# Kernel tuning notes

Measured on AMD Instinct MI355X. Metric: run time of the kernel, lower is better.

The kernel has to match this reference:

```python
import jax, jax.numpy as jnp
import numpy as np

B = 256
NUM_PRIMARY = 32      # cfg.num_primary_caps
PRIM_ATOMS = 8
NUM_CLASSES = 10
DIGIT_ATOMS = 16
NUM_ROUTING = 3       # cfg.num_routing (DigitCap)
IN_DIM = 6 * 6 * NUM_PRIMARY  # 1152
NUM_PIXELS = 28 * 28 * 1


def squash(s, axis):
    # v = ||s||^2/(1+||s||^2) * s/||s||
    n2 = jnp.sum(jnp.square(s), axis=axis, keepdims=True)
    return s * (n2 / (1.0 + n2)) / jnp.sqrt(n2 + 1e-9)


def conv2d(x, w, stride):
    return jax.lax.conv_general_dilated(
        x, w, (stride, stride), 'VALID',
        dimension_numbers=('NCHW', 'OIHW', 'NCHW'))


def setup_inputs() -> dict:
    key = jax.random.key(0)
    ks = jax.random.split(key, 10)
    x = jax.random.uniform(ks[0], (B, 1, 28, 28), jnp.float32)
    labels = jax.random.randint(ks[1], (B,), 0, NUM_CLASSES)
    y = jax.nn.one_hot(labels, NUM_CLASSES, dtype=jnp.float32)
    conv1_w = 0.05 * jax.random.normal(ks[2], (256, 1, 9, 9), jnp.float32)
    conv1_b = jnp.full((256,), 0.1, jnp.float32)
    # primary capsule conv: 256 -> 32 caps * 8 atoms, k=9, s=2 (bias applied after routing)
    prim_w = 0.05 * jax.random.normal(ks[3], (NUM_PRIMARY * PRIM_ATOMS, 256, 9, 9), jnp.float32)
    prim_b = jnp.full((NUM_PRIMARY, PRIM_ATOMS), 0.1, jnp.float32)
    # digit capsule transform: [in_dim, in_atoms, out_dim, out_atoms]
    digit_w = 0.05 * jax.random.normal(ks[4], (IN_DIM, PRIM_ATOMS, NUM_CLASSES, DIGIT_ATOMS), jnp.float32)
    digit_b = jnp.full((NUM_CLASSES, DIGIT_ATOMS), 0.1, jnp.float32)
    w1 = 0.05 * jax.random.normal(ks[5], (NUM_CLASSES * DIGIT_ATOMS, 512), jnp.float32)
    b1 = jnp.zeros((512,), jnp.float32)
    w2 = 0.05 * jax.random.normal(ks[6], (512, 1024), jnp.float32)
    b2 = jnp.zeros((1024,), jnp.float32)
    w3 = 0.05 * jax.random.normal(ks[7], (1024, NUM_PIXELS), jnp.float32)
    b3 = jnp.zeros((NUM_PIXELS,), jnp.float32)
    return dict(x=x, y=y, conv1_w=conv1_w, conv1_b=conv1_b, prim_w=prim_w,
                prim_b=prim_b, digit_w=digit_w, digit_b=digit_b,
                w1=w1, b1=b1, w2=w2, b2=b2, w3=w3, b3=b3)


def reference(x, y, conv1_w, conv1_b, prim_w, prim_b, digit_w, digit_b,
              w1, b1, w2, b2, w3, b3):
    # conv stem
    h = jax.nn.relu(conv2d(x, conv1_w, 1) + conv1_b[None, :, None, None])  # [B,256,20,20]

    # PrimaryCap: conv votes [B, in_dim=1, out=32, atoms=8, 6, 6]; num_routing=1
    votes_p = conv2d(h, prim_w, 2).reshape(B, NUM_PRIMARY, PRIM_ATOMS, 6, 6)
    # one routing iter, input_dim=1: softmax(zeros) over output_dim -> uniform 1/32
    preact_p = votes_p / NUM_PRIMARY + prim_b[None, :, :, None, None]
    caps1 = squash(preact_p, axis=2)  # [B,32,8,6,6]

    # permute(0,1,3,4,2) then flatten -> [B, 1152, 8]
    x3 = jnp.transpose(caps1, (0, 1, 3, 4, 2)).reshape(B, IN_DIM, PRIM_ATOMS)

    # DigitCap votes: [B, in_dim, out_dim, out_atoms]
    votes = jnp.einsum('bia,iaot->biot', x3, digit_w)
    logits = jnp.zeros((B, IN_DIM, NUM_CLASSES), votes.dtype)
    act = None
    for _ in range(NUM_ROUTING):
        route = jax.nn.softmax(logits, axis=2)  # over output capsules
        preact = jnp.einsum('bio,biot->bot', route, votes) + digit_b
        act = squash(preact, axis=-1)  # [B,10,16]
        logits = logits + jnp.einsum('biot,bot->bio', votes, act)
    digit = act

    # Reconstruction: mask by label, 160 -> 512 -> 1024 -> 784
    masked = (digit * y[:, :, None]).reshape(B, NUM_CLASSES * DIGIT_ATOMS)
    r = jax.nn.relu(masked @ w1 + b1)
    r = jax.nn.relu(r @ w2 + b2)
    recon = jax.nn.sigmoid(r @ w3 + b3)
    return digit, recon
```

## Files before the change

kernel.cpp:

```cpp
#include <hip/hip_runtime.h>
#include <hip/hip_bf16.h>

typedef unsigned short u16;
typedef unsigned int u32;

static __device__ __forceinline__ float us2f(u16 u) {
    return __uint_as_float(((u32)u) << 16);
}
static __device__ __forceinline__ u16 f2bu(float f) {
    u32 u = __float_as_uint(f);
    return (u16)((u + 0x7fffu + ((u >> 16) & 1u)) >> 16);
}

typedef __attribute__((ext_vector_type(8))) __bf16 bf16x8;
typedef __attribute__((ext_vector_type(4))) float f32x4;

static __device__ __forceinline__ void async16(const u16* g, u16* l) {
    __builtin_amdgcn_global_load_lds(
        (const __attribute__((address_space(1))) unsigned int*)g,
        (__attribute__((address_space(3))) unsigned int*)l, 16, 0, 0);
}

__global__ void fill_sentinel(float* out, int n, float val) {
    int g = blockIdx.x * 256 + threadIdx.x;
    if (g < n) out[g] = val;
}

__global__ __launch_bounds__(256) void conv_c1wb(const float* __restrict__ w,
                                                 u16* __restrict__ wb)
{
    const int j = blockIdx.x, c = threadIdx.x;
    wb[j * 256 + c] = f2bu(w[c * 81 + j]);
}

__global__ __launch_bounds__(256) void conv1_kernel(const float* __restrict__ x,
    const u16* __restrict__ wb, const float* __restrict__ bias, u16* __restrict__ h)
{
    __shared__ float xs[784];
    __shared__ u16 wl[81 * 256];
    const int b = blockIdx.x >> 2, g = blockIdx.x & 3;
    const int c = threadIdx.x;
    for (int idx = c; idx < 784; idx += 256) xs[idx] = x[b * 784 + idx];
    for (int idx = c; idx < 20736; idx += 256) wl[idx] = wb[idx];
    __syncthreads();
    const float bv = bias[c];
    #pragma unroll 1
    for (int iy = g * 5; iy < g * 5 + 5; ++iy) {
        float acc[20];
        #pragma unroll
        for (int i = 0; i < 20; ++i) acc[i] = bv;
        #pragma unroll 1
        for (int dy = 0; dy < 9; ++dy) {
            float xr[28];
            const float4* xrow = reinterpret_cast<const float4*>(&xs[(iy + dy) * 28]);
            #pragma unroll
            for (int i = 0; i < 7; ++i) {
                float4 v = xrow[i];
                xr[4*i] = v.x; xr[4*i+1] = v.y; xr[4*i+2] = v.z; xr[4*i+3] = v.w;
            }
            #pragma unroll
            for (int dx = 0; dx < 9; ++dx) {
                const float wv = us2f(wl[(dy * 9 + dx) * 256 + c]);
                #pragma unroll
                for (int ix = 0; ix < 20; ++ix) acc[ix] += xr[ix + dx] * wv;
            }
        }
        u16* hp = h + ((b * 20 + iy) * 20) * 256 + c;
        #pragma unroll
        for (int ix = 0; ix < 20; ++ix) hp[ix * 256] = f2bu(fmaxf(acc[ix], 0.f));
    }
}

__global__ __launch_bounds__(256) void transpose_primw(const float* __restrict__ w,
                                                       u16* __restrict__ wt)
{
    __shared__ u16 wl[81 * 258];
    const int n = blockIdx.x, tid = threadIdx.x;
    const float* ws = w + (size_t)n * 20736;
    for (int idx = tid; idx < 20736; idx += 256) {
        const int cc = idx / 81, kk = idx - cc * 81;
        wl[kk * 258 + cc] = f2bu(ws[idx]);
    }
    __syncthreads();
    u16* wo = wt + (size_t)n * 20736;
    for (int q = tid; q < 20736; q += 256)
        wo[q] = wl[(q >> 8) * 258 + (q & 255)];
}

__global__ __launch_bounds__(256) void conv_dwb(const float* __restrict__ dw,
                                                u16* __restrict__ dwb_t)
{
    const int g = blockIdx.x * 256 + threadIdx.x;
    dwb_t[g] = f2bu(dw[g]);
}

__global__ __launch_bounds__(256) void prim_gemm_split(const u16* __restrict__ h,
    const u16* __restrict__ wT, float* __restrict__ pm)
{
    __shared__ u16 As[128 * 32];
    __shared__ u16 Bs[128 * 32];
    const int tid = threadIdx.x;
    const int split = blockIdx.y;
    const int mt = blockIdx.x % 72, nt = blockIdx.x / 72;
    const int mBase = mt * 128, nBase = nt * 128;
    const int tq = tid & 3, tr = tid >> 2;
    const int swzq = tq ^ ((tr >> 1) & 3);
    int m0 = mBase + tr;
    int b0 = m0 / 36, r0 = m0 % 36;
    int aBase0 = ((b0 * 20 + 2 * (r0 / 6)) * 20 + 2 * (r0 % 6)) * 256 + swzq * 8;
    int m1 = m0 + 64;
    int b1 = m1 / 36, r1 = m1 % 36;
    int aBase1 = ((b1 * 20 + 2 * (r1 / 6)) * 20 + 2 * (r1 % 6)) * 256 + swzq * 8;
    const int bBase0 = (nBase + tr) * 20736 + swzq * 8;
    const int bBase1 = (nBase + tr + 64) * 20736 + swzq * 8;
    int kglob = split * 1728;
    int ky = kglob / 2304; int krem = kglob - ky * 2304;
    int kx = krem >> 8; int c0 = krem & 255;

    f32x4 acc[4][4];
    #pragma unroll
    for (int i = 0; i < 4; ++i)
        #pragma unroll
        for (int j = 0; j < 4; ++j) acc[i][j] = (f32x4){0.f, 0.f, 0.f, 0.f};

    const int lane = tid & 63;
    const int wvi = tid >> 6; const int wm = wvi >> 1, wn = wvi & 1;
    const int lcol = lane & 15, lquad = lane >> 4;
    u16* asDst0 = As + wvi * 512;
    u16* asDst1 = As + 2048 + wvi * 512;
    u16* bsDst0 = Bs + wvi * 512;
    u16* bsDst1 = Bs + 2048 + wvi * 512;
    const int rswz = (lquad ^ ((lcol >> 1) & 3)) * 8;
    const u16* Arow = As + (wm * 64 + lcol) * 32 + rswz;
    const u16* Brow = Bs + (wn * 64 + lcol) * 32 + rswz;

    #pragma unroll 1
    for (int kt = 0; kt < 54; ++kt) {
        const int koffA = (ky * 20 + kx) * 256 + c0;
        async16(h + aBase0 + koffA, asDst0);
        async16(h + aBase1 + koffA, asDst1);
        async16(wT + bBase0 + kglob, bsDst0);
        async16(wT + bBase1 + kglob, bsDst1);
        __syncthreads();
        bf16x8 af[4], bfr[4];
        #pragma unroll
        for (int i = 0; i < 4; ++i)
            af[i] = *reinterpret_cast<const bf16x8*>(Arow + i * 512);
        #pragma unroll
        for (int j = 0; j < 4; ++j)
            bfr[j] = *reinterpret_cast<const bf16x8*>(Brow + j * 512);
        #pragma unroll
        for (int i = 0; i < 4; ++i)
            #pragma unroll
            for (int j = 0; j < 4; ++j)
                acc[i][j] = __builtin_amdgcn_mfma_f32_16x16x32_bf16(af[i], bfr[j], acc[i][j], 0, 0, 0);
        kglob += 32; c0 += 32;
        if (c0 == 256) { c0 = 0; if (++kx == 9) { kx = 0; ++ky; } }
        __syncthreads();
    }
    #pragma unroll
    for (int i = 0; i < 4; ++i) {
        const int mrow = mBase + wm * 64 + i * 16 + (lane >> 4) * 4;
        #pragma unroll
        for (int j = 0; j < 4; ++j) {
            const int ncol = nBase + wn * 64 + j * 16 + lcol;
            #pragma unroll
            for (int r = 0; r < 4; ++r)
                unsafeAtomicAdd(&pm[(size_t)(mrow + r) * 256 + ncol], acc[i][j][r]);
        }
    }
}

__global__ __launch_bounds__(256) void squash_kernel(float* __restrict__ pm,
    const float* __restrict__ pb)
{
    const int m = blockIdx.x, t = threadIdx.x;
    float pre = pm[(size_t)m * 256 + t] * (1.f / 32.f) + pb[t];
    float sq = pre * pre;
    sq += __shfl_xor(sq, 1); sq += __shfl_xor(sq, 2); sq += __shfl_xor(sq, 4);
    float scale = (sq / (1.f + sq)) * rsqrtf(sq + 1e-9f);
    pm[(size_t)m * 256 + t] = pre * scale;
}

__global__ __launch_bounds__(192) void votes_gemm(const float* __restrict__ x3m,
    const u16* __restrict__ dwb_t, u16* __restrict__ votes, int hb)
{
    __shared__ float dws[8 * 1280];
    __shared__ float x3s[64 * 64];
    const int ic = blockIdx.x * 8, bc = blockIdx.y * 64;
    const int tid = threadIdx.x;
    for (int q = tid; q < 10240; q += 192)
        dws[q] = us2f(dwb_t[(size_t)ic * 1280 + q]);
    for (int q = tid; q < 4096; q += 192) {
        const int b_l = q >> 6, r = q & 63, i_l = r >> 3, a = r & 7;
        const int i = ic + i_l, cap = i / 36, p = i - cap * 36;
        x3s[q] = x3m[((size_t)(hb + bc + b_l) * 36 + p) * 256 + cap * 8 + a];
    }
    __syncthreads();
    if (tid < 160) {
        const int ot = tid;
        float dwr[8][8];
        #pragma unroll
        for (int i_l = 0; i_l < 8; ++i_l)
            #pragma unroll
            for (int a = 0; a < 8; ++a)
                dwr[i_l][a] = dws[i_l * 1280 + a * 160 + ot];
        #pragma unroll 1
        for (int b_l = 0; b_l < 64; ++b_l) {
            u16 ob[8];
            #pragma unroll
            for (int i_l = 0; i_l < 8; ++i_l) {
                const float* xp = &x3s[b_l * 64 + i_l * 8];
                float v = 0.f;
                #pragma unroll
                for (int a = 0; a < 8; ++a) v += xp[a] * dwr[i_l][a];
                ob[i_l] = f2bu(v);
            }
            uint4 o4;
            o4.x = (u32)ob[0] | ((u32)ob[1] << 16);
            o4.y = (u32)ob[2] | ((u32)ob[3] << 16);
            o4.z = (u32)ob[4] | ((u32)ob[5] << 16);
            o4.w = (u32)ob[6] | ((u32)ob[7] << 16);
            *reinterpret_cast<uint4*>(&votes[((size_t)(bc + b_l) * 160 + ot) * 1152 + ic]) = o4;
        }
    }
}

__global__ __launch_bounds__(256) void routing_act3(const u16* __restrict__ votes,
    const float* __restrict__ logits, float* __restrict__ preactD, int hb, int uniform)
{
    __shared__ float route_s[384 * 10];
    __shared__ float vs[160 * 65];
    const int ic = blockIdx.x * 384, b_l = blockIdx.y;
    const int gb = hb + b_l;
    const int tid = threadIdx.x;
    if (!uniform) {
        for (int q = tid; q < 384; q += 256) {
            const float* lg = &logits[((size_t)gb * 1152 + ic + q) * 10];
            float l[10]; float mx = -1e30f;
            #pragma unroll
            for (int k = 0; k < 10; ++k) { l[k] = lg[k]; mx = fmaxf(mx, l[k]); }
            float s = 0.f;
            #pragma unroll
            for (int k = 0; k < 10; ++k) { l[k] = __expf(l[k] - mx); s += l[k]; }
            const float inv = 1.f / s;
            #pragma unroll
            for (int k = 0; k < 10; ++k) route_s[q * 10 + k] = l[k] * inv;
        }
    }
    float acc = 0.f;
    const int o = (tid & 255) >> 4;
    #pragma unroll 1
    for (int sc = 0; sc < 6; ++sc) {
        __syncthreads();
        for (int q = tid; q < 1280; q += 256) {
            const int ot = q >> 3, i8 = q & 7;
            const uint4 d = *reinterpret_cast<const uint4*>(
                &votes[((size_t)b_l * 160 + ot) * 1152 + ic + sc * 64 + i8 * 8]);
            const u32 du[4] = {d.x, d.y, d.z, d.w};
            float* vp = &vs[ot * 65 + i8 * 8];
            #pragma unroll
            for (int k = 0; k < 4; ++k) {
                vp[2 * k]     = __uint_as_float(du[k] << 16);
                vp[2 * k + 1] = __uint_as_float(du[k] & 0xffff0000u);
            }
        }
        __syncthreads();
        if (tid < 160) {
            const float* vrow = &vs[tid * 65];
            if (uniform) {
                float s = 0.f;
                #pragma unroll
                for (int il = 0; il < 64; ++il) s += vrow[il];
                acc += 0.1f * s;
            } else {
                const float* rp = &route_s[sc * 640 + o];
                #pragma unroll
                for (int il = 0; il < 64; ++il)
                    acc += rp[il * 10] * vrow[il];
            }
        }
    }
    if (tid < 160)
        unsafeAtomicAdd(&preactD[(size_t)gb * 160 + tid], acc);
}

__global__ __launch_bounds__(192) void routing_squash(const float* __restrict__ preactD,
    const float* __restrict__ db, float* __restrict__ act, float* __restrict__ dout, int hb)
{
    const int b = hb + blockIdx.x, tid = threadIdx.x;
    if (tid < 160) {
        float pre = preactD[(size_t)b * 160 + tid] + db[tid];
        float sq = pre * pre;
        sq += __shfl_xor(sq, 1); sq += __shfl_xor(sq, 2);
        sq += __shfl_xor(sq, 4); sq += __shfl_xor(sq, 8);
        float scale = (sq / (1.f + sq)) * rsqrtf(sq + 1e-9f);
        float a = pre * scale;
        act[(size_t)b * 160 + tid] = a;
        if (dout) dout[(size_t)b * 160 + tid] = a;
    }
}

__global__ __launch_bounds__(128) void routing_upd3(const u16* __restrict__ votes,
    const float* __restrict__ act, float* __restrict__ logits, int hb, int first)
{
    __shared__ float act_s[160];
    const int b_l = blockIdx.y, gb = hb + b_l;
    const int i = blockIdx.x * 128 + threadIdx.x;
    for (int q = threadIdx.x; q < 160; q += 128)
        act_s[q] = act[(size_t)gb * 160 + q];
    __syncthreads();
    float acc[10];
    #pragma unroll
    for (int k = 0; k < 10; ++k) acc[k] = 0.f;
    const u16* vb = &votes[(size_t)b_l * 160 * 1152 + i];
    #pragma unroll
    for (int ot = 0; ot < 160; ++ot)
        acc[ot >> 4] += us2f(vb[(size_t)ot * 1152]) * act_s[ot];
    float* lp = &logits[((size_t)gb * 1152 + i) * 10];
    if (first) {
        #pragma unroll
        for (int k = 0; k < 10; ++k) lp[k] = acc[k];
    } else {
        #pragma unroll
        for (int k = 0; k < 10; ++k) lp[k] += acc[k];
    }
}

__global__ __launch_bounds__(256) void mlp_layer(const float* __restrict__ in,
    const float* __restrict__ maskY, const float* __restrict__ w,
    const float* __restrict__ bias, float* __restrict__ outp, int K, int N, int mode)
{
    __shared__ float ins[4 * 1024];
    const int b0 = blockIdx.x * 4;
    const int n = blockIdx.y * 256 + threadIdx.x;
    for (int idx = threadIdx.x; idx < 4 * K; idx += 256) {
        float v = in[(size_t)b0 * K + idx];
        if (maskY) {
            const int b_l = idx / K, j = idx % K;
            v *= maskY[(b0 + b_l) * 10 + (j >> 4)];
        }
        ins[idx] = v;
    }
    __syncthreads();
    if (n < N) {
        float a0 = 0.f, a1 = 0.f, a2 = 0.f, a3 = 0.f;
        for (int k = 0; k < K; ++k) {
            const float wvv = w[(size_t)k * N + n];
            a0 += ins[k] * wvv;
            a1 += ins[K + k] * wvv;
            a2 += ins[2 * K + k] * wvv;
            a3 += ins[3 * K + k] * wvv;
        }
        const float bv = bias[n];
        float v[4] = {a0 + bv, a1 + bv, a2 + bv, a3 + bv};
        #pragma unroll
        for (int j = 0; j < 4; ++j) {
            float xv = v[j];
            xv = (mode == 0) ? fmaxf(xv, 0.f) : 1.f / (1.f + __expf(-xv));
            outp[(size_t)(b0 + j) * N + n] = xv;
        }
    }
}

extern "C" void kernel_launch(void* const* d_in, const int* in_sizes, int n_in,
                              void* d_out, int out_size, void* d_ws, size_t ws_size,
                              hipStream_t stream) {
    const float* x   = (const float*)d_in[0];
    const float* y   = (const float*)d_in[1];
    const float* c1w = (const float*)d_in[2];
    const float* c1b = (const float*)d_in[3];
    const float* pw  = (const float*)d_in[4];
    const float* pb  = (const float*)d_in[5];
    const float* dw  = (const float*)d_in[6];
    const float* db  = (const float*)d_in[7];
    const float* w1  = (const float*)d_in[8];
    const float* b1  = (const float*)d_in[9];
    const float* w2  = (const float*)d_in[10];
    const float* b2  = (const float*)d_in[11];
    const float* w3  = (const float*)d_in[12];
    const float* b3  = (const float*)d_in[13];
    float* out = (float*)d_out;
    char* ws = (char*)d_ws;

    static const int exp_sizes[14] = {200704, 2560, 20736, 256, 5308416, 256,
                                      1474560, 160, 81920, 512, 524288, 1024,
                                      802816, 784};
    int bad = (n_in == 14) ? -1 : -2;
    if (bad == -1)
        for (int i = 0; i < 14; ++i) if (in_sizes[i] != exp_sizes[i]) { bad = i; break; }
    if (bad != -1) {
        fill_sentinel<<<(out_size + 255) / 256, 256, 0, stream>>>(out, out_size,
            7168.f + 16.f * (float)(bad + 1));
        return;
    }
    const size_t NEEDED = 72482816ULL;
    if (ws_size < NEEDED) {
        fill_sentinel<<<(out_size + 255) / 256, 256, 0, stream>>>(out, out_size, 111.0f);
        return;
    }

    u16*   h       = (u16*)(ws);
    u16*   wT2     = (u16*)(ws + 52428800);
    float* x3m     = (float*)(ws + 63045632);
    u16*   c1wb    = (u16*)(ws + 63045632);
    u16*   votes   = (u16*)(ws);
    float* logits  = (float*)(ws + 47185920);
    float* act     = (float*)(ws + 58982400);
    float* preactD = (float*)(ws + 59146240);
    u16*   dwb_t   = (u16*)(ws + 59637760);
    float* r1      = (float*)(ws + 62586880);
    float* r2      = (float*)(ws + 63111168);

    conv_c1wb<<<81, 256, 0, stream>>>(c1w, c1wb);
    conv1_kernel<<<1024, 256, 0, stream>>>(x, c1wb, c1b, h);
    transpose_primw<<<256, 256, 0, stream>>>(pw, wT2);
    hipMemsetAsync(x3m, 0, 9437184, stream);
    prim_gemm_split<<<dim3(144, 12), 256, 0, stream>>>(h, wT2, x3m);
    squash_kernel<<<9216, 256, 0, stream>>>(x3m, pb);
    conv_dwb<<<5760, 256, 0, stream>>>(dw, dwb_t);
    hipMemsetAsync(preactD, 0, 491520, stream);

    float* pD0 = preactD, *pD1 = preactD + 40960, *pD2 = preactD + 81920;
    for (int half = 0; half < 2; ++half) {
        const int hb = half * 128;
        votes_gemm<<<dim3(144, 2), 192, 0, stream>>>(x3m, dwb_t, votes, hb);
        routing_act3<<<dim3(3, 128), 256, 0, stream>>>(votes, logits, pD0, hb, 1);
        routing_squash<<<128, 192, 0, stream>>>(pD0, db, act, (float*)nullptr, hb);
        routing_upd3<<<dim3(9, 128), 128, 0, stream>>>(votes, act, logits, hb, 1);
        routing_act3<<<dim3(3, 128), 256, 0, stream>>>(votes, logits, pD1, hb, 0);
        routing_squash<<<128, 192, 0, stream>>>(pD1, db, act, (float*)nullptr, hb);
        routing_upd3<<<dim3(9, 128), 128, 0, stream>>>(votes, act, logits, hb, 0);
        routing_act3<<<dim3(3, 128), 256, 0, stream>>>(votes, logits, pD2, hb, 0);
        routing_squash<<<128, 192, 0, stream>>>(pD2, db, act, out, hb);
    }

    mlp_layer<<<dim3(64, 2), 256, 0, stream>>>(act, y, w1, b1, r1, 160, 512, 0);
    mlp_layer<<<dim3(64, 4), 256, 0, stream>>>(r1, (float*)nullptr, w2, b2, r2, 512, 1024, 0);
    mlp_layer<<<dim3(64, 4), 256, 0, stream>>>(r2, (float*)nullptr, w3, b3, out + 40960, 1024, 784, 1);
}
```

Before: 778.1 us.

## Double-buffer LDS tiles in primary-caps GEMM to overlap loads with MFMA

The split-K primary capsule GEMM now keeps two LDS stages for A and B. It issues async global-to-LDS loads for the next k-tile before computing the current one, using a partial vmcnt wait and explicit barriers. This hides global load latency behind MFMA work instead of stalling each iteration on its loads. The cost is doubled LDS use per block, which may reduce occupancy, plus hand-placed waitcnt and sched barriers that must stay correct.

```diff
diff --git a/kernel.cpp b/kernel.cpp
--- a/kernel.cpp
+++ b/kernel.cpp
@@ -97,8 +97,8 @@
 __global__ __launch_bounds__(256) void prim_gemm_split(const u16* __restrict__ h,
     const u16* __restrict__ wT, float* __restrict__ pm)
 {
-    __shared__ u16 As[128 * 32];
-    __shared__ u16 Bs[128 * 32];
+    __shared__ u16 As[2 * 4096];
+    __shared__ u16 Bs[2 * 4096];
     const int tid = threadIdx.x;
     const int split = blockIdx.y;
     const int mt = blockIdx.x % 72, nt = blockIdx.x / 72;
@@ -126,41 +126,60 @@
     const int lane = tid & 63;
     const int wvi = tid >> 6; const int wm = wvi >> 1, wn = wvi & 1;
     const int lcol = lane & 15, lquad = lane >> 4;
-    u16* asDst0 = As + wvi * 512;
-    u16* asDst1 = As + 2048 + wvi * 512;
-    u16* bsDst0 = Bs + wvi * 512;
-    u16* bsDst1 = Bs + 2048 + wvi * 512;
+    u16* asD = As + wvi * 512;
+    u16* bsD = Bs + wvi * 512;
     const int rswz = (lquad ^ ((lcol >> 1) & 3)) * 8;
     const u16* Arow = As + (wm * 64 + lcol) * 32 + rswz;
     const u16* Brow = Bs + (wn * 64 + lcol) * 32 + rswz;
 
+    #define STAGE(sel)  do {                                                   \
+        const int koffA = (ky * 20 + kx) * 256 + c0;                           \
+        async16(h + aBase0 + koffA, asD + (sel) * 4096);                       \
+        async16(h + aBase1 + koffA, asD + (sel) * 4096 + 2048);                \
+        async16(wT + bBase0 + kglob, bsD + (sel) * 4096);                      \
+        async16(wT + bBase1 + kglob, bsD + (sel) * 4096 + 2048);               \
+        kglob += 32; c0 += 32;                                                 \
+        if (c0 == 256) { c0 = 0; if (++kx == 9) { kx = 0; ++ky; } }            \
+    } while (0)
+
+    #define COMPUTE(sel)  do {                                                 \
+        bf16x8 af[4], bfr[4];                                                  \
+        _Pragma("unroll")                                                      \
+        for (int i = 0; i < 4; ++i)                                            \
+            af[i] = *reinterpret_cast<const bf16x8*>(Arow + (sel) * 4096 + i * 512); \
+        _Pragma("unroll")                                                      \
+        for (int j = 0; j < 4; ++j)                                            \
+            bfr[j] = *reinterpret_cast<const bf16x8*>(Brow + (sel) * 4096 + j * 512); \
+        _Pragma("unroll")                                                      \
+        for (int i = 0; i < 4; ++i)                                            \
+            _Pragma("unroll")                                                  \
+            for (int j = 0; j < 4; ++j)                                        \
+                acc[i][j] = __builtin_amdgcn_mfma_f32_16x16x32_bf16(af[i], bfr[j], acc[i][j], 0, 0, 0); \
+    } while (0)
+
+    STAGE(0);
     #pragma unroll 1
-    for (int kt = 0; kt < 54; ++kt) {
-        const int koffA = (ky * 20 + kx) * 256 + c0;
-        async16(h + aBase0 + koffA, asDst0);
-        async16(h + aBase1 + koffA, asDst1);
-        async16(wT + bBase0 + kglob, bsDst0);
-        async16(wT + bBase1 + kglob, bsDst1);
-        __syncthreads();
-        bf16x8 af[4], bfr[4];
-        #pragma unroll
-        for (int i = 0; i < 4; ++i)
-            af[i] = *reinterpret_cast<const bf16x8*>(Arow + i * 512);
-        #pragma unroll
-        for (int j = 0; j < 4; ++j)
-            bfr[j] = *reinterpret_cast<const bf16x8*>(Brow + j * 512);
-        #pragma unroll
-        for (int i = 0; i < 4; ++i)
-            #pragma unroll
-            for (int j = 0; j < 4; ++j)
-                acc[i][j] = __builtin_amdgcn_mfma_f32_16x16x32_bf16(af[i], bfr[j], acc[i][j], 0, 0, 0);
-        kglob += 32; c0 += 32;
-        if (c0 == 256) { c0 = 0; if (++kx == 9) { kx = 0; ++ky; } }
-        __syncthreads();
-    }
+    for (int kt = 0; kt < 53; ++kt) {
+        const int sel = kt & 1;
+        STAGE(sel ^ 1);
+        asm volatile("s_waitcnt vmcnt(4)" ::: "memory");
+        __builtin_amdgcn_s_barrier();
+        __builtin_amdgcn_sched_barrier(0);
+        COMPUTE(sel);
+        __builtin_amdgcn_sched_barrier(0);
+        __builtin_amdgcn_s_barrier();
+        __builtin_amdgcn_sched_barrier(0);
+    }
+    asm volatile("s_waitcnt vmcnt(0)" ::: "memory");
+    __builtin_amdgcn_s_barrier();
+    __builtin_amdgcn_sched_barrier(0);
+    COMPUTE(1);
+    #undef STAGE
+    #undef COMPUTE
+
     #pragma unroll
     for (int i = 0; i < 4; ++i) {
-        const int mrow = mBase + wm * 64 + i * 16 + (lane >> 4) * 4;
+        const int mrow = mBase + wm * 64 + i * 16 + lquad * 4;
         #pragma unroll
         for (int j = 0; j < 4; ++j) {
             const int ncol = nBase + wn * 64 + j * 16 + lcol;
```

Result: no change. 784.3 us (+0.8%).
